# Performance work log

Measured on AMD Instinct MI355X. Metric: run time of the kernel, lower is better.

The kernel has to match this reference:

```python
import math
import jax, jax.numpy as jnp
import numpy as np

STREAMS = 4
DIM = 1024
M = 16                      # routing granularity
BUS = STREAMS * DIM         # 4096
C = BUS // M                # 256
SINK_ITERS = 10
SINK_TAU = 0.05
B, L = 4, 2048


def rms_norm(x, gamma):
    # F.normalize(x, dim=-1) * sqrt(dim) * (gamma + 1)
    norm = jnp.sqrt(jnp.sum(x * x, axis=-1, keepdims=True))
    x = x / jnp.maximum(norm, 1e-12)
    return x * jnp.sqrt(jnp.asarray(x.shape[-1], x.dtype)) * (gamma + 1.0)


def sinkhorn_log(logits, num_iters=SINK_ITERS, tau=SINK_TAU):
    n = logits.shape[-1]
    Z = logits / tau
    lm = -math.log(n)
    u = jnp.zeros(Z.shape[:-1], Z.dtype)
    v = jnp.zeros(Z.shape[:-2] + (n,), Z.dtype)
    def body(_, uv):
        u, v = uv
        u = lm - jax.nn.logsumexp(Z + v[..., None, :], axis=-1)
        v = lm - jax.nn.logsumexp(Z + u[..., None], axis=-2)
        return (u, v)
    u, v = jax.lax.fori_loop(0, num_iters, body, (u, v))
    return jnp.exp(Z + u[..., None] + v[..., None, :]) * n


def setup_inputs() -> dict:
    key = jax.random.key(0)
    ks = jax.random.split(key, 8)
    residuals = jax.random.normal(ks[0], (B * STREAMS, L, DIM), jnp.float32)
    branch_output = jax.random.normal(ks[1], (B, L, DIM), jnp.float32)
    gamma = jax.random.normal(ks[2], (BUS,), jnp.float32) * 0.02
    H_res_logits = jnp.full((M, M), -8.0, jnp.float32)
    H_res_logits = H_res_logits.at[jnp.arange(M), jnp.arange(M)].set(0.0)
    phi_res = jax.random.normal(ks[3], (BUS, M * M), jnp.float32) * 0.02
    H_pre_logits = jnp.full((STREAMS,), -8.0, jnp.float32).at[0].set(0.0)
    phi_pre = jax.random.normal(ks[4], (BUS, STREAMS), jnp.float32) * 0.02
    H_post_logits = jnp.zeros((STREAMS,), jnp.float32)
    phi_post = jax.random.normal(ks[5], (BUS, STREAMS), jnp.float32) * 0.02
    a = jnp.asarray(0.01, jnp.float32)
    return dict(residuals=residuals, branch_output=branch_output, gamma=gamma,
                H_res_logits=H_res_logits, phi_res=phi_res, alpha_res=a,
                H_pre_logits=H_pre_logits, phi_pre=phi_pre, alpha_pre=a,
                H_post_logits=H_post_logits, phi_post=phi_post, alpha_post=a)


def reference(residuals, branch_output, gamma, H_res_logits, phi_res, alpha_res,
              H_pre_logits, phi_pre, alpha_pre, H_post_logits, phi_post, alpha_post):
    # (b s) l d -> b l s d
    res = residuals.reshape(B, STREAMS, L, DIM).transpose(0, 2, 1, 3)
    bus = res.reshape(B, L, BUS)
    bus_n = rms_norm(bus, gamma)

    raw = (bus_n @ phi_res).reshape(B, L, M, M)
    S = sinkhorn_log(alpha_res * raw + H_res_logits)
    H_res = S  # no identity mix

    H_pre = jax.nn.softmax(alpha_pre * (bus_n @ phi_pre) + H_pre_logits, axis=-1)
    H_post = jax.nn.softmax(alpha_post * (bus_n @ phi_post) + H_post_logits, axis=-1)

    reshaped = res.reshape(B, L, M, C)
    mixed = jnp.einsum('blst,blsc->bltc', H_res, reshaped).reshape(B, L, STREAMS, DIM)

    branch_input = jnp.einsum('bls,blsd->bld', H_pre, res)

    # depth connection with given branch_output
    branch_to_streams = branch_output[..., None, :] * H_post[..., :, None]
    out = mixed + branch_to_streams            # (B, L, STREAMS, DIM)
    out = out.transpose(0, 2, 1, 3).reshape(B * STREAMS, L, DIM)
    return out, branch_input
```

## Files before the change

kernel.cpp:

```cpp
#include <hip/hip_runtime.h>
#include <hip/hip_bf16.h>
#include <math.h>

#define NSTREAM 4
#define DIM     1024
#define BUSW    4096
#define NTOK    8192
#define NPAD    288
#define KSPLIT  4
#define KCH     1024
#define BM      64
#define BK      32
#define OUT0    ((size_t)16 * 2048 * 1024)

typedef short bf16x8 __attribute__((ext_vector_type(8)));
typedef float f32x4  __attribute__((ext_vector_type(4)));

__device__ __forceinline__ unsigned short f2bf(float f) {
    union { float f; unsigned int u; } x; x.f = f;
    unsigned int r = x.u + 0x7fffu + ((x.u >> 16) & 1u);
    return (unsigned short)(r >> 16);
}
__device__ __forceinline__ unsigned int pack2(float a, float b) {
    return (unsigned int)f2bf(a) | ((unsigned int)f2bf(b) << 16);
}

__global__ void prep_w_kernel(const float* __restrict__ gamma,
                              const float* __restrict__ phi_res,
                              const float* __restrict__ phi_pre,
                              const float* __restrict__ phi_post,
                              unsigned short* __restrict__ W) {
    int idx = blockIdx.x * 256 + threadIdx.x;
    int n = idx >> 12;
    int k = idx & 4095;
    float v = 0.0f;
    if (n < 256)      v = phi_res[k * 256 + n];
    else if (n < 260) v = phi_pre[k * 4 + (n - 256)];
    else if (n < 264) v = phi_post[k * 4 + (n - 260)];
    v *= (gamma[k] + 1.0f);
    W[idx] = f2bf(v);
}

__launch_bounds__(256, 2)
__global__ void gemm_raw_kernel(const float* __restrict__ residuals,
                                const unsigned short* __restrict__ W,
                                float* __restrict__ raw_part) {
    __shared__ unsigned short Alds[BM * BK];
    __shared__ unsigned short Blds[NPAD * BK];

    const int tid = threadIdx.x;
    const int wid = tid >> 6, lane = tid & 63;
    const int tb = blockIdx.x, kc = blockIdx.y;
    const int row0 = tb * BM;

    f32x4 acc[2][9];
#pragma unroll
    for (int i = 0; i < 2; i++)
#pragma unroll
        for (int j = 0; j < 9; j++) acc[i][j] = (f32x4){0.f, 0.f, 0.f, 0.f};

    const int arow = tid >> 2;
    const int akq  = (tid & 3) * 8;
    const int tok  = row0 + arow;
    const int bidx = tok >> 11, lidx = tok & 2047;
    const float* abase = residuals +
        (((size_t)(bidx * 4 + kc) * 2048 + lidx) * 1024 + akq);
    const unsigned short* wbase = W + (size_t)kc * KCH;

    const int fr = lane & 15, hf = lane >> 4;
    const int wr = (wid >> 1) * 32;
    const int wc = (wid & 1) * 144;

    for (int kt = 0; kt < KCH / BK; kt++) {
        const float* ap = abase + kt * BK;
        float4 f0 = *(const float4*)(ap);
        float4 f1 = *(const float4*)(ap + 4);
        uint4 ua;
        ua.x = pack2(f0.x, f0.y); ua.y = pack2(f0.z, f0.w);
        ua.z = pack2(f1.x, f1.y); ua.w = pack2(f1.z, f1.w);
        *(uint4*)&Alds[arow * BK + akq] = ua;
#pragma unroll
        for (int i = 0; i < 5; i++) {
            int idx = i * 256 + tid;
            if (idx < (NPAD * BK) / 8) {
                int rn = idx >> 2, ko = (idx & 3) * 8;
                uint4 w = *(const uint4*)(wbase + (size_t)rn * BUSW + kt * BK + ko);
                *(uint4*)&Blds[rn * BK + ko] = w;
            }
        }
        __syncthreads();

        bf16x8 afrag[2], bfrag[9];
#pragma unroll
        for (int mt = 0; mt < 2; mt++)
            afrag[mt] = *(const bf16x8*)&Alds[(wr + mt * 16 + fr) * BK + hf * 8];
#pragma unroll
        for (int nt = 0; nt < 9; nt++)
            bfrag[nt] = *(const bf16x8*)&Blds[(wc + nt * 16 + fr) * BK + hf * 8];
#pragma unroll
        for (int mt = 0; mt < 2; mt++)
#pragma unroll
            for (int nt = 0; nt < 9; nt++)
                acc[mt][nt] = __builtin_amdgcn_mfma_f32_16x16x32_bf16(
                    afrag[mt], bfrag[nt], acc[mt][nt], 0, 0, 0);
        __syncthreads();
    }

#pragma unroll
    for (int mt = 0; mt < 2; mt++)
#pragma unroll
        for (int nt = 0; nt < 9; nt++)
#pragma unroll
            for (int r = 0; r < 4; r++) {
                int token = row0 + wr + mt * 16 + hf * 4 + r;
                int col   = wc + nt * 16 + fr;
                raw_part[((size_t)kc * NTOK + token) * NPAD + col] = acc[mt][nt][r];
            }
}

__global__ void fused_tail_kernel(const float* __restrict__ residuals,
                                  const float* __restrict__ branch_output,
                                  const float* __restrict__ H_res_logits,
                                  const float* __restrict__ alpha_res_p,
                                  const float* __restrict__ H_pre_logits,
                                  const float* __restrict__ alpha_pre_p,
                                  const float* __restrict__ H_post_logits,
                                  const float* __restrict__ alpha_post_p,
                                  const float* __restrict__ raw_part,
                                  float* __restrict__ out) {
    const int t = blockIdx.x;
    const int b = t >> 11, l = t & 2047;
    const int tid = threadIdx.x;
    const int wid = tid >> 6, lane = tid & 63;

    __shared__ float busf[4096];
    __shared__ float Zl[256];
    __shared__ float uu[16], vv[16];
    __shared__ float extra[8];
    __shared__ float hpre[4], hpost[4];
    __shared__ float redbuf[4];
    __shared__ float scale_sh;

    const float* rbase = residuals + ((size_t)b * 4 * 2048 + l) * 1024;
    float sumsq = 0.f;
#pragma unroll
    for (int s = 0; s < 4; s++) {
        float4 v = *(const float4*)(rbase + (size_t)s * 2048 * 1024 + tid * 4);
        *(float4*)&busf[s * 1024 + tid * 4] = v;
        sumsq += v.x * v.x + v.y * v.y + v.z * v.z + v.w * v.w;
    }
#pragma unroll
    for (int off = 32; off > 0; off >>= 1) sumsq += __shfl_down(sumsq, off, 64);
    if (lane == 0) redbuf[wid] = sumsq;
    __syncthreads();
    if (tid == 0) {
        float ss = redbuf[0] + redbuf[1] + redbuf[2] + redbuf[3];
        scale_sh = 64.0f / fmaxf(sqrtf(ss), 1e-12f);
    }
    __syncthreads();
    const float scale = scale_sh;

    const float a_res = alpha_res_p[0];
    float rsum = 0.f;
#pragma unroll
    for (int kc = 0; kc < 4; kc++)
        rsum += raw_part[((size_t)kc * NTOK + t) * NPAD + tid];
    Zl[tid] = (a_res * scale * rsum + H_res_logits[tid]) * (1.0f / 0.05f);
    if (tid < 8) {
        float es = 0.f;
#pragma unroll
        for (int kc = 0; kc < 4; kc++)
            es += raw_part[((size_t)kc * NTOK + t) * NPAD + 256 + tid];
        extra[tid] = es;
    }
    if (tid < 16) vv[tid] = 0.f;
    __syncthreads();

    if (tid == 0) {
        float apre = alpha_pre_p[0], apost = alpha_post_p[0];
        float pv[4], qv[4], pm = -3e38f, qm = -3e38f;
        for (int s = 0; s < 4; s++) {
            pv[s] = apre  * scale * extra[s]     + H_pre_logits[s];
            qv[s] = apost * scale * extra[4 + s] + H_post_logits[s];
            pm = fmaxf(pm, pv[s]); qm = fmaxf(qm, qv[s]);
        }
        float ps = 0.f, qs = 0.f;
        for (int s = 0; s < 4; s++) {
            pv[s] = __expf(pv[s] - pm); qv[s] = __expf(qv[s] - qm);
            ps += pv[s]; qs += qv[s];
        }
        for (int s = 0; s < 4; s++) { hpre[s] = pv[s] / ps; hpost[s] = qv[s] / qs; }
    }

    const float lm = -2.772588722239781f;
    for (int it = 0; it < 10; it++) {
        if (tid < 16) {
            int r = tid; float m = -3e38f;
            for (int c = 0; c < 16; c++) m = fmaxf(m, Zl[r * 16 + c] + vv[c]);
            float s2 = 0.f;
            for (int c = 0; c < 16; c++) s2 += __expf(Zl[r * 16 + c] + vv[c] - m);
            uu[r] = lm - (m + __logf(s2));
        }
        __syncthreads();
        if (tid < 16) {
            int c = tid; float m = -3e38f;
            for (int r = 0; r < 16; r++) m = fmaxf(m, Zl[r * 16 + c] + uu[r]);
            float s2 = 0.f;
            for (int r = 0; r < 16; r++) s2 += __expf(Zl[r * 16 + c] + uu[r] - m);
            vv[c] = lm - (m + __logf(s2));
        }
        __syncthreads();
    }
    Zl[tid] = __expf(Zl[tid] + uu[tid >> 4] + vv[tid & 15]) * 16.0f;
    __syncthreads();

    float busr[16];
#pragma unroll
    for (int s = 0; s < 16; s++) busr[s] = busf[s * 256 + tid];
    const float* bo = branch_output + ((size_t)b * 2048 + l) * 1024;
#pragma unroll
    for (int tc = 0; tc < 16; tc++) {
        float acc2 = 0.f;
#pragma unroll
        for (int s = 0; s < 16; s++) acc2 += Zl[s * 16 + tc] * busr[s];
        int sout = tc >> 2, d = (tc & 3) * 256 + tid;
        float val = acc2 + bo[d] * hpost[sout];
        out[((size_t)(b * 4 + sout) * 2048 + l) * 1024 + d] = val;
    }

    int d0 = tid * 4;
    float4 bi; bi.x = bi.y = bi.z = bi.w = 0.f;
#pragma unroll
    for (int s = 0; s < 4; s++) {
        float4 v = *(const float4*)&busf[s * 1024 + d0];
        float h = hpre[s];
        bi.x += h * v.x; bi.y += h * v.y; bi.z += h * v.z; bi.w += h * v.w;
    }
    *(float4*)&out[OUT0 + ((size_t)b * 2048 + l) * 1024 + d0] = bi;
}

extern "C" void kernel_launch(void* const* d_in, const int* in_sizes, int n_in,
                              void* d_out, int out_size, void* d_ws, size_t ws_size,
                              hipStream_t stream) {
    const float* residuals  = (const float*)d_in[0];
    const float* branch_out = (const float*)d_in[1];
    const float* gamma      = (const float*)d_in[2];
    const float* H_res_log  = (const float*)d_in[3];
    const float* phi_res    = (const float*)d_in[4];
    const float* alpha_res  = (const float*)d_in[5];
    const float* H_pre_log  = (const float*)d_in[6];
    const float* phi_pre    = (const float*)d_in[7];
    const float* alpha_pre  = (const float*)d_in[8];
    const float* H_post_log = (const float*)d_in[9];
    const float* phi_post   = (const float*)d_in[10];
    const float* alpha_post = (const float*)d_in[11];

    unsigned short* W = (unsigned short*)d_ws;
    float* raw_part = (float*)((char*)d_ws + (size_t)NPAD * BUSW * 2);
    float* out = (float*)d_out;

    hipLaunchKernelGGL(prep_w_kernel, dim3(NPAD * BUSW / 256), dim3(256), 0, stream,
                       gamma, phi_res, phi_pre, phi_post, W);
    hipLaunchKernelGGL(gemm_raw_kernel, dim3(NTOK / BM, KSPLIT), dim3(256), 0, stream,
                       residuals, W, raw_part);
    hipLaunchKernelGGL(fused_tail_kernel, dim3(NTOK), dim3(256), 0, stream,
                       residuals, branch_out, H_res_log, alpha_res,
                       H_pre_log, alpha_pre, H_post_log, alpha_post, raw_part, out);
}
```

Baseline: 430.7 us.

## Map one token per wavefront in tail kernel; prefetch and pad GEMM LDS tiles

The tail kernel now handles one token per 64-lane wavefront. Bus data, the Sinkhorn matrix and the softmax weights stay in registers, and reductions use shuffles in place of shared memory and block barriers. This removes the serial 16-thread Sinkhorn loop and its __syncthreads. The GEMM kernel register-prefetches the next K tile's A and B data while computing the current one, and pads the LDS row stride to 40 to reduce bank conflicts. The cost is higher register pressure from 16 float4 bus registers per lane and a heavier shuffle count in the mixing loop.

```diff
diff --git a/kernel.cpp b/kernel.cpp
--- a/kernel.cpp
+++ b/kernel.cpp
@@ -11,6 +11,7 @@
 #define KCH     1024
 #define BM      64
 #define BK      32
+#define LDA     40
 #define OUT0    ((size_t)16 * 2048 * 1024)
 
 typedef short bf16x8 __attribute__((ext_vector_type(8)));
@@ -45,8 +46,8 @@
 __global__ void gemm_raw_kernel(const float* __restrict__ residuals,
                                 const unsigned short* __restrict__ W,
                                 float* __restrict__ raw_part) {
-    __shared__ unsigned short Alds[BM * BK];
-    __shared__ unsigned short Blds[NPAD * BK];
+    __shared__ unsigned short Alds[BM * LDA];
+    __shared__ unsigned short Blds[NPAD * LDA];
 
     const int tid = threadIdx.x;
     const int wid = tid >> 6, lane = tid & 63;
@@ -71,32 +72,51 @@
     const int wr = (wid >> 1) * 32;
     const int wc = (wid & 1) * 144;
 
+    int brn[5], bko[5];
+#pragma unroll
+    for (int i = 0; i < 5; i++) {
+        int idx = i * 256 + tid;
+        brn[i] = idx >> 2; bko[i] = (idx & 3) * 8;
+    }
+
+    float4 pf0, pf1;
+    uint4 pb[5];
+    pf0 = *(const float4*)(abase);
+    pf1 = *(const float4*)(abase + 4);
+#pragma unroll
+    for (int i = 0; i < 5; i++)
+        if (i * 256 + tid < (NPAD * BK) / 8)
+            pb[i] = *(const uint4*)(wbase + (size_t)brn[i] * BUSW + bko[i]);
+
     for (int kt = 0; kt < KCH / BK; kt++) {
-        const float* ap = abase + kt * BK;
-        float4 f0 = *(const float4*)(ap);
-        float4 f1 = *(const float4*)(ap + 4);
         uint4 ua;
-        ua.x = pack2(f0.x, f0.y); ua.y = pack2(f0.z, f0.w);
-        ua.z = pack2(f1.x, f1.y); ua.w = pack2(f1.z, f1.w);
-        *(uint4*)&Alds[arow * BK + akq] = ua;
-#pragma unroll
-        for (int i = 0; i < 5; i++) {
-            int idx = i * 256 + tid;
-            if (idx < (NPAD * BK) / 8) {
-                int rn = idx >> 2, ko = (idx & 3) * 8;
-                uint4 w = *(const uint4*)(wbase + (size_t)rn * BUSW + kt * BK + ko);
-                *(uint4*)&Blds[rn * BK + ko] = w;
-            }
-        }
+        ua.x = pack2(pf0.x, pf0.y); ua.y = pack2(pf0.z, pf0.w);
+        ua.z = pack2(pf1.x, pf1.y); ua.w = pack2(pf1.z, pf1.w);
+        *(uint4*)&Alds[arow * LDA + akq] = ua;
+#pragma unroll
+        for (int i = 0; i < 5; i++)
+            if (i * 256 + tid < (NPAD * BK) / 8)
+                *(uint4*)&Blds[brn[i] * LDA + bko[i]] = pb[i];
         __syncthreads();
 
+        if (kt + 1 < KCH / BK) {
+            const float* ap = abase + (kt + 1) * BK;
+            pf0 = *(const float4*)(ap);
+            pf1 = *(const float4*)(ap + 4);
+#pragma unroll
+            for (int i = 0; i < 5; i++)
+                if (i * 256 + tid < (NPAD * BK) / 8)
+                    pb[i] = *(const uint4*)(wbase + (size_t)brn[i] * BUSW +
+                                            (kt + 1) * BK + bko[i]);
+        }
+
         bf16x8 afrag[2], bfrag[9];
 #pragma unroll
         for (int mt = 0; mt < 2; mt++)
-            afrag[mt] = *(const bf16x8*)&Alds[(wr + mt * 16 + fr) * BK + hf * 8];
+            afrag[mt] = *(const bf16x8*)&Alds[(wr + mt * 16 + fr) * LDA + hf * 8];
 #pragma unroll
         for (int nt = 0; nt < 9; nt++)
-            bfrag[nt] = *(const bf16x8*)&Blds[(wc + nt * 16 + fr) * BK + hf * 8];
+            bfrag[nt] = *(const bf16x8*)&Blds[(wc + nt * 16 + fr) * LDA + hf * 8];
 #pragma unroll
         for (int mt = 0; mt < 2; mt++)
 #pragma unroll
@@ -118,6 +138,7 @@
             }
 }
 
+__launch_bounds__(256, 4)
 __global__ void fused_tail_kernel(const float* __restrict__ residuals,
                                   const float* __restrict__ branch_output,
                                   const float* __restrict__ H_res_logits,
@@ -128,115 +149,133 @@
                                   const float* __restrict__ alpha_post_p,
                                   const float* __restrict__ raw_part,
                                   float* __restrict__ out) {
-    const int t = blockIdx.x;
-    const int b = t >> 11, l = t & 2047;
-    const int tid = threadIdx.x;
-    const int wid = tid >> 6, lane = tid & 63;
-
-    __shared__ float busf[4096];
-    __shared__ float Zl[256];
-    __shared__ float uu[16], vv[16];
-    __shared__ float extra[8];
-    __shared__ float hpre[4], hpost[4];
-    __shared__ float redbuf[4];
-    __shared__ float scale_sh;
-
-    const float* rbase = residuals + ((size_t)b * 4 * 2048 + l) * 1024;
+    const int wid = threadIdx.x >> 6, lane = threadIdx.x & 63;
+    const int t = blockIdx.x * 4 + wid;
+    const int b = t >> 11, lt = t & 2047;
+
+    const float* rbase = residuals + ((size_t)b * 4 * 2048 + lt) * 1024;
+    float4 busr[16];
     float sumsq = 0.f;
 #pragma unroll
-    for (int s = 0; s < 4; s++) {
-        float4 v = *(const float4*)(rbase + (size_t)s * 2048 * 1024 + tid * 4);
-        *(float4*)&busf[s * 1024 + tid * 4] = v;
-        sumsq += v.x * v.x + v.y * v.y + v.z * v.z + v.w * v.w;
-    }
-#pragma unroll
-    for (int off = 32; off > 0; off >>= 1) sumsq += __shfl_down(sumsq, off, 64);
-    if (lane == 0) redbuf[wid] = sumsq;
-    __syncthreads();
-    if (tid == 0) {
-        float ss = redbuf[0] + redbuf[1] + redbuf[2] + redbuf[3];
-        scale_sh = 64.0f / fmaxf(sqrtf(ss), 1e-12f);
-    }
-    __syncthreads();
-    const float scale = scale_sh;
+    for (int s = 0; s < 4; s++)
+#pragma unroll
+        for (int q = 0; q < 4; q++) {
+            float4 v = *(const float4*)(rbase + (size_t)s * 2048 * 1024 + q * 256 + lane * 4);
+            busr[s * 4 + q] = v;
+            sumsq += v.x * v.x + v.y * v.y + v.z * v.z + v.w * v.w;
+        }
+#pragma unroll
+    for (int m = 1; m < 64; m <<= 1) sumsq += __shfl_xor(sumsq, m, 64);
+    const float scale = 64.0f / fmaxf(sqrtf(sumsq), 1e-12f);
+
+    float4 zr = {0.f, 0.f, 0.f, 0.f}, ep = {0.f, 0.f, 0.f, 0.f}, eq = {0.f, 0.f, 0.f, 0.f};
+#pragma unroll
+    for (int kc = 0; kc < 4; kc++) {
+        const float* p = raw_part + ((size_t)kc * NTOK + t) * NPAD;
+        float4 a = *(const float4*)(p + lane * 4);
+        zr.x += a.x; zr.y += a.y; zr.z += a.z; zr.w += a.w;
+        float4 e0 = *(const float4*)(p + 256);
+        float4 e1 = *(const float4*)(p + 260);
+        ep.x += e0.x; ep.y += e0.y; ep.z += e0.z; ep.w += e0.w;
+        eq.x += e1.x; eq.y += e1.y; eq.z += e1.z; eq.w += e1.w;
+    }
 
     const float a_res = alpha_res_p[0];
-    float rsum = 0.f;
-#pragma unroll
-    for (int kc = 0; kc < 4; kc++)
-        rsum += raw_part[((size_t)kc * NTOK + t) * NPAD + tid];
-    Zl[tid] = (a_res * scale * rsum + H_res_logits[tid]) * (1.0f / 0.05f);
-    if (tid < 8) {
-        float es = 0.f;
-#pragma unroll
-        for (int kc = 0; kc < 4; kc++)
-            es += raw_part[((size_t)kc * NTOK + t) * NPAD + 256 + tid];
-        extra[tid] = es;
-    }
-    if (tid < 16) vv[tid] = 0.f;
-    __syncthreads();
-
-    if (tid == 0) {
-        float apre = alpha_pre_p[0], apost = alpha_post_p[0];
-        float pv[4], qv[4], pm = -3e38f, qm = -3e38f;
-        for (int s = 0; s < 4; s++) {
-            pv[s] = apre  * scale * extra[s]     + H_pre_logits[s];
-            qv[s] = apost * scale * extra[4 + s] + H_post_logits[s];
-            pm = fmaxf(pm, pv[s]); qm = fmaxf(qm, qv[s]);
-        }
+    float4 hres = *(const float4*)(H_res_logits + lane * 4);
+    float Z[4];
+    Z[0] = (a_res * scale * zr.x + hres.x) * 20.0f;
+    Z[1] = (a_res * scale * zr.y + hres.y) * 20.0f;
+    Z[2] = (a_res * scale * zr.z + hres.z) * 20.0f;
+    Z[3] = (a_res * scale * zr.w + hres.w) * 20.0f;
+
+    float hpre[4], hpost[4];
+    {
+        const float apre = alpha_pre_p[0], apost = alpha_post_p[0];
+        float4 hpl = *(const float4*)(H_pre_logits);
+        float4 hql = *(const float4*)(H_post_logits);
+        float pv[4] = { apre * scale * ep.x + hpl.x, apre * scale * ep.y + hpl.y,
+                        apre * scale * ep.z + hpl.z, apre * scale * ep.w + hpl.w };
+        float qv[4] = { apost * scale * eq.x + hql.x, apost * scale * eq.y + hql.y,
+                        apost * scale * eq.z + hql.z, apost * scale * eq.w + hql.w };
+        float pm = fmaxf(fmaxf(pv[0], pv[1]), fmaxf(pv[2], pv[3]));
+        float qm = fmaxf(fmaxf(qv[0], qv[1]), fmaxf(qv[2], qv[3]));
         float ps = 0.f, qs = 0.f;
+#pragma unroll
         for (int s = 0; s < 4; s++) {
             pv[s] = __expf(pv[s] - pm); qv[s] = __expf(qv[s] - qm);
             ps += pv[s]; qs += qv[s];
         }
+#pragma unroll
         for (int s = 0; s < 4; s++) { hpre[s] = pv[s] / ps; hpost[s] = qv[s] / qs; }
     }
 
     const float lm = -2.772588722239781f;
+    float vv[4] = {0.f, 0.f, 0.f, 0.f};
+    float u = 0.f;
+#pragma unroll
     for (int it = 0; it < 10; it++) {
-        if (tid < 16) {
-            int r = tid; float m = -3e38f;
-            for (int c = 0; c < 16; c++) m = fmaxf(m, Zl[r * 16 + c] + vv[c]);
-            float s2 = 0.f;
-            for (int c = 0; c < 16; c++) s2 += __expf(Zl[r * 16 + c] + vv[c] - m);
-            uu[r] = lm - (m + __logf(s2));
-        }
-        __syncthreads();
-        if (tid < 16) {
-            int c = tid; float m = -3e38f;
-            for (int r = 0; r < 16; r++) m = fmaxf(m, Zl[r * 16 + c] + uu[r]);
-            float s2 = 0.f;
-            for (int r = 0; r < 16; r++) s2 += __expf(Zl[r * 16 + c] + uu[r] - m);
-            vv[c] = lm - (m + __logf(s2));
-        }
-        __syncthreads();
-    }
-    Zl[tid] = __expf(Zl[tid] + uu[tid >> 4] + vv[tid & 15]) * 16.0f;
-    __syncthreads();
-
-    float busr[16];
-#pragma unroll
-    for (int s = 0; s < 16; s++) busr[s] = busf[s * 256 + tid];
-    const float* bo = branch_output + ((size_t)b * 2048 + l) * 1024;
-#pragma unroll
-    for (int tc = 0; tc < 16; tc++) {
-        float acc2 = 0.f;
-#pragma unroll
-        for (int s = 0; s < 16; s++) acc2 += Zl[s * 16 + tc] * busr[s];
-        int sout = tc >> 2, d = (tc & 3) * 256 + tid;
-        float val = acc2 + bo[d] * hpost[sout];
-        out[((size_t)(b * 4 + sout) * 2048 + l) * 1024 + d] = val;
-    }
-
-    int d0 = tid * 4;
-    float4 bi; bi.x = bi.y = bi.z = bi.w = 0.f;
-#pragma unroll
-    for (int s = 0; s < 4; s++) {
-        float4 v = *(const float4*)&busf[s * 1024 + d0];
-        float h = hpre[s];
-        bi.x += h * v.x; bi.y += h * v.y; bi.z += h * v.z; bi.w += h * v.w;
-    }
-    *(float4*)&out[OUT0 + ((size_t)b * 2048 + l) * 1024 + d0] = bi;
+        float m0 = fmaxf(fmaxf(Z[0] + vv[0], Z[1] + vv[1]),
+                         fmaxf(Z[2] + vv[2], Z[3] + vv[3]));
+        m0 = fmaxf(m0, __shfl_xor(m0, 1, 64));
+        m0 = fmaxf(m0, __shfl_xor(m0, 2, 64));
+        float s0 = __expf(Z[0] + vv[0] - m0) + __expf(Z[1] + vv[1] - m0) +
+                   __expf(Z[2] + vv[2] - m0) + __expf(Z[3] + vv[3] - m0);
+        s0 += __shfl_xor(s0, 1, 64);
+        s0 += __shfl_xor(s0, 2, 64);
+        u = lm - (m0 + __logf(s0));
+        float cm[4], cs[4];
+#pragma unroll
+        for (int j = 0; j < 4; j++) cm[j] = Z[j] + u;
+#pragma unroll
+        for (int msk = 4; msk < 64; msk <<= 1)
+#pragma unroll
+            for (int j = 0; j < 4; j++) cm[j] = fmaxf(cm[j], __shfl_xor(cm[j], msk, 64));
+#pragma unroll
+        for (int j = 0; j < 4; j++) cs[j] = __expf(Z[j] + u - cm[j]);
+#pragma unroll
+        for (int msk = 4; msk < 64; msk <<= 1)
+#pragma unroll
+            for (int j = 0; j < 4; j++) cs[j] += __shfl_xor(cs[j], msk, 64);
+#pragma unroll
+        for (int j = 0; j < 4; j++) vv[j] = lm - (cm[j] + __logf(cs[j]));
+    }
+    float S[4];
+#pragma unroll
+    for (int j = 0; j < 4; j++) S[j] = __expf(Z[j] + u + vv[j]) * 16.0f;
+
+    const float* bob = branch_output + ((size_t)b * 2048 + lt) * 1024;
+    float* outb = out;
+#pragma unroll
+    for (int q = 0; q < 4; q++) {
+        float4 bv = *(const float4*)(bob + q * 256 + lane * 4);
+#pragma unroll
+        for (int so = 0; so < 4; so++) {
+            float4 acc;
+            float hp = hpost[so];
+            acc.x = hp * bv.x; acc.y = hp * bv.y; acc.z = hp * bv.z; acc.w = hp * bv.w;
+#pragma unroll
+            for (int n = 0; n < 16; n++) {
+                float sv = __shfl(S[q], n * 4 + so, 64);
+                float4 bu = busr[n];
+                acc.x += sv * bu.x; acc.y += sv * bu.y;
+                acc.z += sv * bu.z; acc.w += sv * bu.w;
+            }
+            *(float4*)(outb + ((size_t)(b * 4 + so) * 2048 + lt) * 1024 +
+                       q * 256 + lane * 4) = acc;
+        }
+    }
+
+#pragma unroll
+    for (int q = 0; q < 4; q++) {
+        float4 bi = {0.f, 0.f, 0.f, 0.f};
+#pragma unroll
+        for (int s = 0; s < 4; s++) {
+            float4 v = busr[s * 4 + q];
+            float h = hpre[s];
+            bi.x += h * v.x; bi.y += h * v.y; bi.z += h * v.z; bi.w += h * v.w;
+        }
+        *(float4*)(outb + OUT0 + ((size_t)b * 2048 + lt) * 1024 + q * 256 + lane * 4) = bi;
+    }
 }
 
 extern "C" void kernel_launch(void* const* d_in, const int* in_sizes, int n_in,
@@ -263,7 +302,7 @@
                        gamma, phi_res, phi_pre, phi_post, W);
     hipLaunchKernelGGL(gemm_raw_kernel, dim3(NTOK / BM, KSPLIT), dim3(256), 0, stream,
                        residuals, W, raw_part);
-    hipLaunchKernelGGL(fused_tail_kernel, dim3(NTOK), dim3(256), 0, stream,
+    hipLaunchKernelGGL(fused_tail_kernel, dim3(NTOK / 4), dim3(256), 0, stream,
                        residuals, branch_out, H_res_log, alpha_res,
                        H_pre_log, alpha_pre, H_post_log, alpha_post, raw_part, out);
 }
```

Result: slower. 491.2 us (+14.0%).
